# Kernel optimization log

Measured on AMD Instinct MI355X. Metric: run time of the kernel, lower is better.

Reference implementation:

```python
import jax, jax.numpy as jnp
import numpy as np

N = 50000      # num_nodes
E = 400000     # num_edges
HDIM = 256     # h_dim
H = 4          # num_heads
D = HDIM // H  # per-head dim
NEG_SLOPE = 0.2  # DGL GATConv default leaky-relu slope


def setup_inputs() -> dict:
    key = jax.random.key(0)
    ks = jax.random.split(key, 12)
    sw = 1.0 / np.sqrt(HDIM)   # fan-in scaling for fc weights
    sa = 1.0 / np.sqrt(D)      # scaling for attention vectors
    return {
        "nids": jnp.arange(N, dtype=jnp.int32),
        "edge_src": jax.random.randint(ks[0], (E,), 0, N, dtype=jnp.int32),
        "edge_dst": jax.random.randint(ks[1], (E,), 0, N, dtype=jnp.int32),
        "emb": jax.random.normal(ks[2], (N, HDIM), jnp.float32),
        "W1": jax.random.normal(ks[3], (HDIM, HDIM), jnp.float32) * sw,
        "al1": jax.random.normal(ks[4], (H, D), jnp.float32) * sa,
        "ar1": jax.random.normal(ks[5], (H, D), jnp.float32) * sa,
        "b1": jnp.zeros((HDIM,), jnp.float32),
        "W2": jax.random.normal(ks[6], (HDIM, HDIM), jnp.float32) * sw,
        "al2": jax.random.normal(ks[7], (H, D), jnp.float32) * sa,
        "ar2": jax.random.normal(ks[8], (H, D), jnp.float32) * sa,
        "b2": jnp.zeros((HDIM,), jnp.float32),
    }


def _gat_layer(x, src, dst, W, al, ar, b):
    # DGL GATConv: fc -> per-head attn logits -> edge softmax over dst -> scatter-add
    f = (x @ W).reshape(-1, H, D)                       # [N,H,D]
    el = jnp.einsum('nhd,hd->nh', f, al)                # [N,H]
    er = jnp.einsum('nhd,hd->nh', f, ar)                # [N,H]
    e = jax.nn.leaky_relu(el[src] + er[dst], NEG_SLOPE) # [E,H]
    # segment softmax over incoming edges of each dst node
    m = jax.ops.segment_max(e, dst, num_segments=N)     # [N,H] (-inf for empty)
    ex = jnp.exp(e - m[dst])                            # [E,H]
    s = jax.ops.segment_sum(ex, dst, num_segments=N)    # [N,H]
    alpha = ex / s[dst]                                 # [E,H]
    msg = alpha[:, :, None] * f[src]                    # [E,H,D]
    out = jax.ops.segment_sum(msg, dst, num_segments=N) # [N,H,D]
    return out + b.reshape(1, H, D)


def reference(nids, edge_src, edge_dst, emb, W1, al1, ar1, b1, W2, al2, ar2, b2):
    x = emb[nids]                                        # embedding lookup [N,HDIM]
    h = _gat_layer(x, edge_src, edge_dst, W1, al1, ar1, b1)  # [N,H,D]
    h = jax.nn.elu(h)
    h = h.reshape(-1, HDIM)                              # concat heads for layer 2
    out = _gat_layer(h, edge_src, edge_dst, W2, al2, ar2, b2)  # [N,H,D]
    return out  # dropout is identity at inference
```

## Files before the change

kernel.cpp:

```cpp
#include <hip/hip_runtime.h>
#include <math.h>

#define NN 50000
#define EE 400000
#define HD 256
#define NH 4
#define DH 64
#define NEG_SLOPE 0.2f

typedef __attribute__((ext_vector_type(8))) __bf16 bf16x8;
typedef __attribute__((ext_vector_type(4))) float f32x4;

__device__ __forceinline__ float bf2f(unsigned short h) {
  return __uint_as_float(((unsigned)h) << 16);
}

__global__ void k_zero_i32(int* __restrict__ p, int n) {
  int i = blockIdx.x * blockDim.x + threadIdx.x;
  if (i < n) p[i] = 0;
}

__global__ void k_count(const int* __restrict__ dst, int* __restrict__ counts,
                        int* __restrict__ rank) {
  int e = blockIdx.x * blockDim.x + threadIdx.x;
  if (e < EE) rank[e] = atomicAdd(&counts[dst[e]], 1);
}

__global__ void k_scan1(const int* __restrict__ counts, int* __restrict__ row_ptr,
                        int* __restrict__ bsums) {
  __shared__ int sm[256];
  int i = blockIdx.x * 256 + threadIdx.x;
  int v = (i < NN) ? counts[i] : 0;
  sm[threadIdx.x] = v;
  __syncthreads();
  for (int off = 1; off < 256; off <<= 1) {
    int t = (threadIdx.x >= off) ? sm[threadIdx.x - off] : 0;
    __syncthreads();
    sm[threadIdx.x] += t;
    __syncthreads();
  }
  if (i < NN) row_ptr[i + 1] = sm[threadIdx.x];
  if (threadIdx.x == 255) bsums[blockIdx.x] = sm[255];
}

__global__ void k_scan2(int* __restrict__ bsums, int nb) {
  __shared__ int sm[256];
  int v = (threadIdx.x < nb) ? bsums[threadIdx.x] : 0;
  sm[threadIdx.x] = v;
  __syncthreads();
  for (int off = 1; off < 256; off <<= 1) {
    int t = (threadIdx.x >= off) ? sm[threadIdx.x - off] : 0;
    __syncthreads();
    sm[threadIdx.x] += t;
    __syncthreads();
  }
  if (threadIdx.x < nb) bsums[threadIdx.x] = sm[threadIdx.x] - v;
}

__global__ void k_scan3(int* __restrict__ row_ptr, const int* __restrict__ bsums) {
  int i = blockIdx.x * 256 + threadIdx.x;
  if (i < NN) row_ptr[i + 1] += bsums[blockIdx.x];
  if (blockIdx.x == 0 && threadIdx.x == 0) row_ptr[0] = 0;
}

__global__ void k_scatter(const int* __restrict__ src, const int* __restrict__ dst,
                          const int* __restrict__ row_ptr, const int* __restrict__ rank,
                          int* __restrict__ csr_src) {
  int e = blockIdx.x * blockDim.x + threadIdx.x;
  if (e < EE) csr_src[row_ptr[dst[e]] + rank[e]] = src[e];
}

__global__ __launch_bounds__(256) void k_prep_w2(const float* __restrict__ W1,
                                                 const float* __restrict__ W2,
                                                 __bf16* __restrict__ W1H,
                                                 __bf16* __restrict__ W1L,
                                                 __bf16* __restrict__ W2H,
                                                 __bf16* __restrict__ W2L) {
  int b = blockIdx.x;
  const float* W = (b < 256) ? W1 : W2;
  __bf16* WH = (b < 256) ? W1H : W2H;
  __bf16* WL = (b < 256) ? W1L : W2L;
  int t = (b & 255) * 256 + threadIdx.x;
  int n = t & 255, k = t >> 8;
  float x = W[(size_t)k * 256 + n];
  __bf16 h = (__bf16)x;
  size_t o = (size_t)(k >> 5) * 8192 + (size_t)((k >> 3) & 3) * 2048 + (size_t)n * 8 + (k & 7);
  WH[o] = h;
  WL[o] = (__bf16)(x - (float)h);
}

__device__ __forceinline__ void gload_lds16(const void* g, void* l) {
  __builtin_amdgcn_global_load_lds((const __attribute__((address_space(1))) void*)g,
                                   (__attribute__((address_space(3))) void*)l, 16, 0, 0);
}

__global__ __launch_bounds__(256) void k_gemm_mfma(
    const float* __restrict__ A, const int* __restrict__ idx,
    const __bf16* __restrict__ WtH, const __bf16* __restrict__ WtL,
    const float* __restrict__ al, const float* __restrict__ ar,
    __bf16* __restrict__ C, float* __restrict__ el, float* __restrict__ er,
    int Mrows) {
  __shared__ bf16x8 AsH[4 * 64];
  __shared__ bf16x8 AsL[4 * 64];
  __shared__ bf16x8 BsH[4 * 256];
  __shared__ bf16x8 BsL[4 * 256];

  int tid = threadIdx.x;
  int lane = tid & 63;
  int w = tid >> 6;
  int row0 = blockIdx.x * 64;

  f32x4 acc[4][4];
#pragma unroll
  for (int i = 0; i < 4; ++i)
#pragma unroll
    for (int j = 0; j < 4; ++j) acc[i][j] = (f32x4){0.f, 0.f, 0.f, 0.f};

  int s_khalf = tid & 3;
  int s_row = tid >> 2;
  int garow = row0 + s_row;
  bool valid = garow < Mrows;
  int arow = valid ? (idx ? idx[garow] : garow) : 0;
  const float* aptr = A + (size_t)arow * HD + s_khalf * 8;

  int khalf = lane >> 4;
  int l15 = lane & 15;

  float x[8];
  if (valid) {
    *(float4*)&x[0] = *(const float4*)(aptr);
    *(float4*)&x[4] = *(const float4*)(aptr + 4);
  } else {
#pragma unroll
    for (int i = 0; i < 8; ++i) x[i] = 0.f;
  }
#pragma unroll
  for (int j = 0; j < 4; ++j) {
    int chunk = w * 4 + j;
    size_t goff = ((size_t)chunk * 64 + lane) * 8;
    gload_lds16(WtH + goff, (void*)&BsH[chunk * 64]);
    gload_lds16(WtL + goff, (void*)&BsL[chunk * 64]);
  }
  {
    bf16x8 hv, lv;
#pragma unroll
    for (int i = 0; i < 8; ++i) {
      __bf16 h = (__bf16)x[i];
      hv[i] = h;
      lv[i] = (__bf16)(x[i] - (float)h);
    }
    AsH[s_khalf * 64 + s_row] = hv;
    AsL[s_khalf * 64 + s_row] = lv;
  }
  __syncthreads();

  for (int kb = 0; kb < 8; ++kb) {
    bf16x8 ah[4], alo[4], bh[4], blo[4];
#pragma unroll
    for (int mf = 0; mf < 4; ++mf) {
      ah[mf] = AsH[khalf * 64 + mf * 16 + l15];
      alo[mf] = AsL[khalf * 64 + mf * 16 + l15];
    }
#pragma unroll
    for (int nf = 0; nf < 4; ++nf) {
      int n = w * 64 + nf * 16 + l15;
      bh[nf] = BsH[khalf * 256 + n];
      blo[nf] = BsL[khalf * 256 + n];
    }
    __syncthreads();

    if (kb < 7) {
      if (valid) {
        *(float4*)&x[0] = *(const float4*)(aptr + (kb + 1) * 32);
        *(float4*)&x[4] = *(const float4*)(aptr + (kb + 1) * 32 + 4);
      }
#pragma unroll
      for (int j = 0; j < 4; ++j) {
        int chunk = w * 4 + j;
        size_t goff = (size_t)(kb + 1) * 8192 + ((size_t)chunk * 64 + lane) * 8;
        gload_lds16(WtH + goff, (void*)&BsH[chunk * 64]);
        gload_lds16(WtL + goff, (void*)&BsL[chunk * 64]);
      }
    }

#pragma unroll
    for (int mf = 0; mf < 4; ++mf)
#pragma unroll
      for (int nf = 0; nf < 4; ++nf) {
        acc[mf][nf] = __builtin_amdgcn_mfma_f32_16x16x32_bf16(ah[mf], bh[nf], acc[mf][nf], 0, 0, 0);
        acc[mf][nf] = __builtin_amdgcn_mfma_f32_16x16x32_bf16(ah[mf], blo[nf], acc[mf][nf], 0, 0, 0);
        acc[mf][nf] = __builtin_amdgcn_mfma_f32_16x16x32_bf16(alo[mf], bh[nf], acc[mf][nf], 0, 0, 0);
      }

    if (kb < 7) {
      bf16x8 hv, lv;
#pragma unroll
      for (int i = 0; i < 8; ++i) {
        __bf16 h = (__bf16)x[i];
        hv[i] = h;
        lv[i] = (__bf16)(x[i] - (float)h);
      }
      AsH[s_khalf * 64 + s_row] = hv;
      AsL[s_khalf * 64 + s_row] = lv;
    }
    __syncthreads();
  }

  float alv[4], arv[4];
#pragma unroll
  for (int nf = 0; nf < 4; ++nf) {
    alv[nf] = al[w * 64 + nf * 16 + l15];
    arv[nf] = ar[w * 64 + nf * 16 + l15];
  }
#pragma unroll
  for (int mf = 0; mf < 4; ++mf) {
#pragma unroll
    for (int r = 0; r < 4; ++r) {
      int row = row0 + mf * 16 + (lane >> 4) * 4 + r;
      bool rv = row < Mrows;
      float se = 0.f, sr = 0.f;
#pragma unroll
      for (int nf = 0; nf < 4; ++nf) {
        float v = acc[mf][nf][r];
        se = fmaf(v, alv[nf], se);
        sr = fmaf(v, arv[nf], sr);
        if (rv) C[(size_t)row * HD + w * 64 + nf * 16 + l15] = (__bf16)v;
      }
#pragma unroll
      for (int off = 1; off < 16; off <<= 1) {
        se += __shfl_xor(se, off);
        sr += __shfl_xor(sr, off);
      }
      if (rv && l15 == 0) {
        el[row * NH + w] = se;
        er[row * NH + w] = sr;
      }
    }
  }
}

__global__ __launch_bounds__(256) void k_aggregate(const __bf16* __restrict__ f,
                                                   const float* __restrict__ el,
                                                   const float* __restrict__ er,
                                                   const int* __restrict__ row_ptr,
                                                   const int* __restrict__ csr_src,
                                                   const float* __restrict__ bias,
                                                   float* __restrict__ out, int act) {
  int node = blockIdx.x * 4 + (threadIdx.x >> 6);
  if (node >= NN) return;
  int lane = threadIdx.x & 63;
  int start = row_ptr[node];
  int deg = row_ptr[node + 1] - start;

  float ern = er[node * NH + (lane & 3)];

  int sreg[4];
  float ereg[4];
  float mloc = -INFINITY;
#pragma unroll
  for (int c = 0; c < 4; ++c) {
    int j = c * 16 + (lane >> 2);
    int s = 0;
    float e = -INFINITY;
    if (c * 16 < deg && j < deg) {
      s = csr_src[start + j];
      e = el[s * NH + (lane & 3)] + ern;
      e = (e >= 0.f) ? e : NEG_SLOPE * e;
    }
    sreg[c] = s;
    ereg[c] = e;
    mloc = fmaxf(mloc, e);
  }
  for (int j0 = 64; j0 < deg; j0 += 16) {
    int j = j0 + (lane >> 2);
    if (j < deg) {
      int s = csr_src[start + j];
      float e = el[s * NH + (lane & 3)] + ern;
      e = (e >= 0.f) ? e : NEG_SLOPE * e;
      mloc = fmaxf(mloc, e);
    }
  }
  float mm = mloc;
#pragma unroll
  for (int off = 4; off < 64; off <<= 1) mm = fmaxf(mm, __shfl_xor(mm, off));

  float vreg[4];
  float vloc = 0.f;
#pragma unroll
  for (int c = 0; c < 4; ++c) {
    float v = (ereg[c] > -INFINITY) ? __expf(ereg[c] - mm) : 0.f;
    vreg[c] = v;
    vloc += v;
  }
  for (int j0 = 64; j0 < deg; j0 += 16) {
    int j = j0 + (lane >> 2);
    if (j < deg) {
      int s = csr_src[start + j];
      float e = el[s * NH + (lane & 3)] + ern;
      e = (e >= 0.f) ? e : NEG_SLOPE * e;
      vloc += __expf(e - mm);
    }
  }
  float ss = vloc;
#pragma unroll
  for (int off = 4; off < 64; off <<= 1) ss += __shfl_xor(ss, off);

  float inv_own = (ss > 0.f) ? (1.f / ss) : 0.f;
  float areg[4];
#pragma unroll
  for (int c = 0; c < 4; ++c) areg[c] = vreg[c] * inv_own;

  int head = lane >> 4;

  float4 acc = ((const float4*)bias)[lane];
  for (int c = 0; c < 4; ++c) {
    int base = c * 16;
    if (base >= deg) break;
    int cnt = deg - base;
    cnt = (cnt > 16) ? 16 : cnt;
    for (int g = 0; g < cnt; g += 8) {
      ushort4 u[8];
      float aa[8];
#pragma unroll
      for (int jj = 0; jj < 8; ++jj) {
        int j = g + jj;
        int jc = (j < cnt) ? j : (cnt - 1);
        int srcl = jc * 4 + head;
        int s = __shfl(sreg[c], srcl);
        float a = __shfl(areg[c], srcl);
        aa[jj] = (j < cnt) ? a : 0.f;
        u[jj] = ((const ushort4*)(f + (size_t)s * HD))[lane];
      }
#pragma unroll
      for (int jj = 0; jj < 8; ++jj) {
        acc.x = fmaf(aa[jj], bf2f(u[jj].x), acc.x);
        acc.y = fmaf(aa[jj], bf2f(u[jj].y), acc.y);
        acc.z = fmaf(aa[jj], bf2f(u[jj].z), acc.z);
        acc.w = fmaf(aa[jj], bf2f(u[jj].w), acc.w);
      }
    }
  }
  if (deg > 64) {
    float mH = __shfl(mm, head);
    float sH = __shfl(ss, head);
    float erH = __shfl(ern, head);
    float invH = (sH > 0.f) ? (1.f / sH) : 0.f;
    for (int j = 64; j < deg; ++j) {
      int s = csr_src[start + j];
      float e = el[s * NH + head] + erH;
      e = (e >= 0.f) ? e : NEG_SLOPE * e;
      float a = __expf(e - mH) * invH;
      ushort4 u = ((const ushort4*)(f + (size_t)s * HD))[lane];
      acc.x = fmaf(a, bf2f(u.x), acc.x);
      acc.y = fmaf(a, bf2f(u.y), acc.y);
      acc.z = fmaf(a, bf2f(u.z), acc.z);
      acc.w = fmaf(a, bf2f(u.w), acc.w);
    }
  }

  if (act) {
    acc.x = (acc.x > 0.f) ? acc.x : __expf(acc.x) - 1.f;
    acc.y = (acc.y > 0.f) ? acc.y : __expf(acc.y) - 1.f;
    acc.z = (acc.z > 0.f) ? acc.z : __expf(acc.z) - 1.f;
    acc.w = (acc.w > 0.f) ? acc.w : __expf(acc.w) - 1.f;
  }
  ((float4*)(out + (size_t)node * HD))[lane] = acc;
}

extern "C" void kernel_launch(void* const* d_in, const int* in_sizes, int n_in,
                              void* d_out, int out_size, void* d_ws, size_t ws_size,
                              hipStream_t stream) {
  const int* nids = (const int*)d_in[0];
  const int* esrc = (const int*)d_in[1];
  const int* edst = (const int*)d_in[2];
  const float* emb = (const float*)d_in[3];
  const float* W1 = (const float*)d_in[4];
  const float* al1 = (const float*)d_in[5];
  const float* ar1 = (const float*)d_in[6];
  const float* b1 = (const float*)d_in[7];
  const float* W2 = (const float*)d_in[8];
  const float* al2 = (const float*)d_in[9];
  const float* ar2 = (const float*)d_in[10];
  const float* b2 = (const float*)d_in[11];
  float* out = (float*)d_out;

  char* w = (char*)d_ws;
  size_t off = 0;
  __bf16* fbuf = (__bf16*)(w + off); off += (size_t)NN * HD * 2;
  float* el = (float*)(w + off); off += (size_t)NN * NH * 4;
  float* er = (float*)(w + off); off += (size_t)NN * NH * 4;
  int* row_ptr = (int*)(w + off); off += (size_t)(NN + 1) * 4;
  int* counts = (int*)(w + off); off += (size_t)NN * 4;
  int* rank = (int*)(w + off); off += (size_t)EE * 4;
  int* csr_src = (int*)(w + off); off += (size_t)EE * 4;
  int* bsums = (int*)(w + off); off += 1024;
  __bf16* W1tH = (__bf16*)(w + off); off += (size_t)HD * HD * 2;
  __bf16* W1tL = (__bf16*)(w + off); off += (size_t)HD * HD * 2;
  __bf16* W2tH = (__bf16*)(w + off); off += (size_t)HD * HD * 2;
  __bf16* W2tL = (__bf16*)(w + off); off += (size_t)HD * HD * 2;

  int nbN = (NN + 255) / 256;
  int nbE = (EE + 255) / 256;

  k_zero_i32<<<nbN, 256, 0, stream>>>(counts, NN);
  k_count<<<nbE, 256, 0, stream>>>(edst, counts, rank);
  k_scan1<<<nbN, 256, 0, stream>>>(counts, row_ptr, bsums);
  k_scan2<<<1, 256, 0, stream>>>(bsums, nbN);
  k_scan3<<<nbN, 256, 0, stream>>>(row_ptr, bsums);
  k_scatter<<<nbE, 256, 0, stream>>>(esrc, edst, row_ptr, rank, csr_src);
  k_prep_w2<<<512, 256, 0, stream>>>(W1, W2, W1tH, W1tL, W2tH, W2tL);

  int gemm_grid = (NN + 63) / 64;
  int nbNode4 = (NN + 3) / 4;

  k_gemm_mfma<<<gemm_grid, 256, 0, stream>>>(emb, nids, W1tH, W1tL, al1, ar1,
                                             fbuf, el, er, NN);
  k_aggregate<<<nbNode4, 256, 0, stream>>>(fbuf, el, er, row_ptr, csr_src, b1, out, 1);

  k_gemm_mfma<<<gemm_grid, 256, 0, stream>>>(out, nullptr, W2tH, W2tL, al2, ar2,
                                             fbuf, el, er, NN);
  k_aggregate<<<nbNode4, 256, 0, stream>>>(fbuf, el, er, row_ptr, csr_src, b2, out, 0);
}
```

Baseline: 199.2 us.

## Load GEMM operands directly from global into registers, dropping LDS staging

The MFMA GEMM no longer stages A and B tiles through shared memory with global_load_lds and barriers. Each lane now loads its bf16 hi/lo weight fragments and fp32 A rows straight from global memory, splitting A to bf16 in registers. This removes the per-iteration __syncthreads and LDS round trips. The cost is redundant global and L2 traffic, because every wave reloads A rows and B fragments. Workspace buffers are also aligned to 256 bytes.

After: 229.3 us. +15.1%, slower.

```diff
diff --git a/kernel.cpp b/kernel.cpp
--- a/kernel.cpp
+++ b/kernel.cpp
@@ -89,100 +89,59 @@
   WL[o] = (__bf16)(x - (float)h);
 }
 
-__device__ __forceinline__ void gload_lds16(const void* g, void* l) {
-  __builtin_amdgcn_global_load_lds((const __attribute__((address_space(1))) void*)g,
-                                   (__attribute__((address_space(3))) void*)l, 16, 0, 0);
-}
-
 __global__ __launch_bounds__(256) void k_gemm_mfma(
     const float* __restrict__ A, const int* __restrict__ idx,
     const __bf16* __restrict__ WtH, const __bf16* __restrict__ WtL,
     const float* __restrict__ al, const float* __restrict__ ar,
     __bf16* __restrict__ C, float* __restrict__ el, float* __restrict__ er,
     int Mrows) {
-  __shared__ bf16x8 AsH[4 * 64];
-  __shared__ bf16x8 AsL[4 * 64];
-  __shared__ bf16x8 BsH[4 * 256];
-  __shared__ bf16x8 BsL[4 * 256];
-
   int tid = threadIdx.x;
   int lane = tid & 63;
   int w = tid >> 6;
   int row0 = blockIdx.x * 64;
-
-  f32x4 acc[4][4];
-#pragma unroll
-  for (int i = 0; i < 4; ++i)
-#pragma unroll
-    for (int j = 0; j < 4; ++j) acc[i][j] = (f32x4){0.f, 0.f, 0.f, 0.f};
-
-  int s_khalf = tid & 3;
-  int s_row = tid >> 2;
-  int garow = row0 + s_row;
-  bool valid = garow < Mrows;
-  int arow = valid ? (idx ? idx[garow] : garow) : 0;
-  const float* aptr = A + (size_t)arow * HD + s_khalf * 8;
-
   int khalf = lane >> 4;
   int l15 = lane & 15;
 
-  float x[8];
-  if (valid) {
-    *(float4*)&x[0] = *(const float4*)(aptr);
-    *(float4*)&x[4] = *(const float4*)(aptr + 4);
-  } else {
-#pragma unroll
-    for (int i = 0; i < 8; ++i) x[i] = 0.f;
-  }
-#pragma unroll
-  for (int j = 0; j < 4; ++j) {
-    int chunk = w * 4 + j;
-    size_t goff = ((size_t)chunk * 64 + lane) * 8;
-    gload_lds16(WtH + goff, (void*)&BsH[chunk * 64]);
-    gload_lds16(WtL + goff, (void*)&BsL[chunk * 64]);
-  }
-  {
-    bf16x8 hv, lv;
-#pragma unroll
-    for (int i = 0; i < 8; ++i) {
-      __bf16 h = (__bf16)x[i];
-      hv[i] = h;
-      lv[i] = (__bf16)(x[i] - (float)h);
-    }
-    AsH[s_khalf * 64 + s_row] = hv;
-    AsL[s_khalf * 64 + s_row] = lv;
-  }
-  __syncthreads();
-
+  f32x4 acc[4][4];
+#pragma unroll
+  for (int i = 0; i < 4; ++i)
+#pragma unroll
+    for (int j = 0; j < 4; ++j) acc[i][j] = (f32x4){0.f, 0.f, 0.f, 0.f};
+
+  const float* ap[4];
+#pragma unroll
+  for (int mf = 0; mf < 4; ++mf) {
+    int r = row0 + mf * 16 + l15;
+    r = (r < Mrows) ? r : (Mrows - 1);
+    int arow = idx ? idx[r] : r;
+    ap[mf] = A + (size_t)arow * HD + khalf * 8;
+  }
+  const __bf16* bhbase = WtH + (size_t)khalf * 2048 + ((size_t)w * 64 + l15) * 8;
+  const __bf16* blbase = WtL + (size_t)khalf * 2048 + ((size_t)w * 64 + l15) * 8;
+
+#pragma unroll 2
   for (int kb = 0; kb < 8; ++kb) {
     bf16x8 ah[4], alo[4], bh[4], blo[4];
 #pragma unroll
+    for (int nf = 0; nf < 4; ++nf) {
+      bh[nf] = *(const bf16x8*)(bhbase + (size_t)kb * 8192 + nf * 128);
+      blo[nf] = *(const bf16x8*)(blbase + (size_t)kb * 8192 + nf * 128);
+    }
+#pragma unroll
     for (int mf = 0; mf < 4; ++mf) {
-      ah[mf] = AsH[khalf * 64 + mf * 16 + l15];
-      alo[mf] = AsL[khalf * 64 + mf * 16 + l15];
-    }
-#pragma unroll
-    for (int nf = 0; nf < 4; ++nf) {
-      int n = w * 64 + nf * 16 + l15;
-      bh[nf] = BsH[khalf * 256 + n];
-      blo[nf] = BsL[khalf * 256 + n];
-    }
-    __syncthreads();
-
-    if (kb < 7) {
-      if (valid) {
-        *(float4*)&x[0] = *(const float4*)(aptr + (kb + 1) * 32);
-        *(float4*)&x[4] = *(const float4*)(aptr + (kb + 1) * 32 + 4);
-      }
-#pragma unroll
-      for (int j = 0; j < 4; ++j) {
-        int chunk = w * 4 + j;
-        size_t goff = (size_t)(kb + 1) * 8192 + ((size_t)chunk * 64 + lane) * 8;
-        gload_lds16(WtH + goff, (void*)&BsH[chunk * 64]);
-        gload_lds16(WtL + goff, (void*)&BsL[chunk * 64]);
-      }
-    }
-
+      float xx[8];
+      *(float4*)&xx[0] = *(const float4*)(ap[mf] + kb * 32);
+      *(float4*)&xx[4] = *(const float4*)(ap[mf] + kb * 32 + 4);
+      bf16x8 hv, lv;
+#pragma unroll
+      for (int i = 0; i < 8; ++i) {
+        __bf16 h = (__bf16)xx[i];
+        hv[i] = h;
+        lv[i] = (__bf16)(xx[i] - (float)h);
+      }
+      ah[mf] = hv;
+      alo[mf] = lv;
+    }
 #pragma unroll
     for (int mf = 0; mf < 4; ++mf)
 #pragma unroll
@@ -191,19 +150,6 @@
         acc[mf][nf] = __builtin_amdgcn_mfma_f32_16x16x32_bf16(ah[mf], blo[nf], acc[mf][nf], 0, 0, 0);
         acc[mf][nf] = __builtin_amdgcn_mfma_f32_16x16x32_bf16(alo[mf], bh[nf], acc[mf][nf], 0, 0, 0);
       }
-
-    if (kb < 7) {
-      bf16x8 hv, lv;
-#pragma unroll
-      for (int i = 0; i < 8; ++i) {
-        __bf16 h = (__bf16)x[i];
-        hv[i] = h;
-        lv[i] = (__bf16)(x[i] - (float)h);
-      }
-      AsH[s_khalf * 64 + s_row] = hv;
-      AsL[s_khalf * 64 + s_row] = lv;
-    }
-    __syncthreads();
   }
 
   float alv[4], arv[4];
@@ -386,18 +332,23 @@
 
   char* w = (char*)d_ws;
   size_t off = 0;
-  __bf16* fbuf = (__bf16*)(w + off); off += (size_t)NN * HD * 2;
-  float* el = (float*)(w + off); off += (size_t)NN * NH * 4;
-  float* er = (float*)(w + off); off += (size_t)NN * NH * 4;
-  int* row_ptr = (int*)(w + off); off += (size_t)(NN + 1) * 4;
-  int* counts = (int*)(w + off); off += (size_t)NN * 4;
-  int* rank = (int*)(w + off); off += (size_t)EE * 4;
-  int* csr_src = (int*)(w + off); off += (size_t)EE * 4;
-  int* bsums = (int*)(w + off); off += 1024;
-  __bf16* W1tH = (__bf16*)(w + off); off += (size_t)HD * HD * 2;
-  __bf16* W1tL = (__bf16*)(w + off); off += (size_t)HD * HD * 2;
-  __bf16* W2tH = (__bf16*)(w + off); off += (size_t)HD * HD * 2;
-  __bf16* W2tL = (__bf16*)(w + off); off += (size_t)HD * HD * 2;
+  auto alloc = [&](size_t bytes) {
+    void* p = w + off;
+    off += (bytes + 255) & ~(size_t)255;
+    return p;
+  };
+  __bf16* fbuf = (__bf16*)alloc((size_t)NN * HD * 2);
+  float* el = (float*)alloc((size_t)NN * NH * 4);
+  float* er = (float*)alloc((size_t)NN * NH * 4);
+  int* row_ptr = (int*)alloc((size_t)(NN + 1) * 4);
+  int* counts = (int*)alloc((size_t)NN * 4);
+  int* rank = (int*)alloc((size_t)EE * 4);
+  int* csr_src = (int*)alloc((size_t)EE * 4);
+  int* bsums = (int*)alloc(1024);
+  __bf16* W1tH = (__bf16*)alloc((size_t)HD * HD * 2);
+  __bf16* W1tL = (__bf16*)alloc((size_t)HD * HD * 2);
+  __bf16* W2tH = (__bf16*)alloc((size_t)HD * HD * 2);
+  __bf16* W2tL = (__bf16*)alloc((size_t)HD * HD * 2);
 
   int nbN = (NN + 255) / 256;
   int nbE = (EE + 255) / 256;
```
